# Performance work log

Measured on AMD Instinct MI355X. Metric: run time of the kernel, lower is better.

Reference implementation:

```python
import jax, jax.numpy as jnp
import numpy as np


def setup_inputs() -> dict:
    key = jax.random.key(0)
    k1, k2, k3 = jax.random.split(key, 3)
    B, Cin, Cout, K, H, W = 32, 128, 128, 4, 112, 112
    x = jax.random.normal(k1, (B, Cin, H, W), dtype=jnp.float32)
    # Conv2d 1x1 weights: [K, out_ch, in_ch] (kernel dims of size 1 squeezed)
    expert_w = jax.random.normal(k2, (K, Cout, Cin), dtype=jnp.float32) * (1.0 / np.sqrt(Cin))
    gate_w = jax.random.normal(k3, (K, Cin), dtype=jnp.float32) * (1.0 / np.sqrt(Cin))
    gate_b = jnp.zeros((K,), dtype=jnp.float32)
    return {"x": x, "expert_w": expert_w, "gate_w": gate_w, "gate_b": gate_b}


def reference(x, expert_w, gate_w, gate_b):
    # Gate: global average pool -> 1x1 conv -> softmax over K
    pooled = jnp.mean(x, axis=(2, 3))                      # [B, Cin]
    logits = pooled @ gate_w.T + gate_b                    # [B, K]
    g = jax.nn.softmax(logits, axis=1)                     # [B, K]
    # Combine expert weights per sample (math-equivalent to sum_k g_k * conv_k(x))
    w_b = jnp.einsum('bk,koi->boi', g, expert_w)           # [B, Cout, Cin]
    out = jnp.einsum('boi,bihw->bohw', w_b, x)             # [B, Cout, H, W]
    return out
```

## Files before the change

### kernel.cpp

```cpp
#include <hip/hip_runtime.h>
#include <hip/hip_bf16.h>
#include <stdint.h>

#define B_    32
#define CIN   128
#define COUT  128
#define KEXP  4
#define HW_   12544

typedef __attribute__((ext_vector_type(8))) short bf16x8;
typedef __attribute__((ext_vector_type(4))) float f32x4;

static __device__ __forceinline__ ushort f2bf(float f) {
    uint32_t u = __builtin_bit_cast(uint32_t, f);
    u += 0x7FFFu + ((u >> 16) & 1u);
    return (ushort)(u >> 16);
}

__global__ __launch_bounds__(256) void pool_kernel(const float* __restrict__ x,
                                                   float* __restrict__ pooled) {
    const int row = blockIdx.x;
    const float4* __restrict__ x4 = (const float4*)(x + (size_t)row * HW_);
    const int t = threadIdx.x;
    float s = 0.f;
    for (int idx = t; idx < HW_ / 4; idx += 256) {
        float4 v = x4[idx];
        s += (v.x + v.y) + (v.z + v.w);
    }
    #pragma unroll
    for (int off = 32; off > 0; off >>= 1) s += __shfl_down(s, off, 64);
    __shared__ float wsum[4];
    if ((t & 63) == 0) wsum[t >> 6] = s;
    __syncthreads();
    if (t == 0) pooled[row] = (wsum[0] + wsum[1] + wsum[2] + wsum[3]) * (1.0f / HW_);
}

__global__ __launch_bounds__(256) void gate_kernel(const float* __restrict__ pooled,
                                                   const float* __restrict__ gate_w,
                                                   const float* __restrict__ gate_b,
                                                   const float* __restrict__ expert_w,
                                                   short* __restrict__ wmix) {
    const int b = blockIdx.x;
    const int t = threadIdx.x;
    const int wid = t >> 6, lane = t & 63;
    __shared__ float logits[KEXP];
    __shared__ float gsh[KEXP];
    {
        float p0 = pooled[b * CIN + lane];
        float p1 = pooled[b * CIN + 64 + lane];
        float s = p0 * gate_w[wid * CIN + lane] + p1 * gate_w[wid * CIN + 64 + lane];
        #pragma unroll
        for (int off = 32; off > 0; off >>= 1) s += __shfl_down(s, off, 64);
        if (lane == 0) logits[wid] = s + gate_b[wid];
    }
    __syncthreads();
    if (t == 0) {
        float m = fmaxf(fmaxf(logits[0], logits[1]), fmaxf(logits[2], logits[3]));
        float e0 = expf(logits[0] - m), e1 = expf(logits[1] - m);
        float e2 = expf(logits[2] - m), e3 = expf(logits[3] - m);
        float inv = 1.f / (e0 + e1 + e2 + e3);
        gsh[0] = e0 * inv; gsh[1] = e1 * inv; gsh[2] = e2 * inv; gsh[3] = e3 * inv;
    }
    __syncthreads();
    const float g0 = gsh[0], g1 = gsh[1], g2 = gsh[2], g3 = gsh[3];
    for (int idx = t; idx < COUT * CIN; idx += 256) {
        float w = g0 * expert_w[idx]
                + g1 * expert_w[COUT * CIN + idx]
                + g2 * expert_w[2 * COUT * CIN + idx]
                + g3 * expert_w[3 * COUT * CIN + idx];
        wmix[b * COUT * CIN + idx] = (short)f2bf(w);
    }
}

__global__ __launch_bounds__(256) void conv_kernel(const float* __restrict__ x,
                                                   const short* __restrict__ wmix,
                                                   float* __restrict__ out) {
    __shared__ char wlds[COUT * 256];
    __shared__ char xlds[64 * 256];
    const int b  = blockIdx.y;
    const int p0 = blockIdx.x * 64;
    const int t  = threadIdx.x;

    {
        const uint4* __restrict__ wsrc = (const uint4*)(wmix + (size_t)b * COUT * CIN);
        #pragma unroll
        for (int pass = 0; pass < 8; ++pass) {
            int o  = (t >> 4) + pass * 16;
            int i4 = t & 15;
            uint4 v = wsrc[o * 16 + i4];
            int byte = (o * 256 + i4 * 16) ^ ((o & 7) << 4);
            *(uint4*)(wlds + byte) = v;
        }
    }

    {
        const int pg = t & 15;
        const int cg = t >> 4;
        #pragma unroll
        for (int p = 0; p < 2; ++p) {
            const int cin0 = p * 64 + cg * 4;
            const float* xrow = x + (size_t)b * CIN * HW_ + (size_t)cin0 * HW_ + p0 + pg * 4;
            float va[4][4];
            #pragma unroll
            for (int i = 0; i < 4; ++i) {
                float4 v = *(const float4*)(xrow + (size_t)i * HW_);
                va[i][0] = v.x; va[i][1] = v.y; va[i][2] = v.z; va[i][3] = v.w;
            }
            #pragma unroll
            for (int j = 0; j < 4; ++j) {
                const int pix = pg * 4 + j;
                uint32_t lo = (uint32_t)f2bf(va[0][j]) | ((uint32_t)f2bf(va[1][j]) << 16);
                uint32_t hi = (uint32_t)f2bf(va[2][j]) | ((uint32_t)f2bf(va[3][j]) << 16);
                int byte = (pix * 256 + cin0 * 2) ^ ((pix & 7) << 4);
                uint2 w2; w2.x = lo; w2.y = hi;
                *(uint2*)(xlds + byte) = w2;
            }
        }
    }

    const int wave = t >> 6;
    const int lane = t & 63;
    const int n = lane & 15;
    const int h = lane >> 4;

    __syncthreads();

    bf16x8 xfrag[4];
    {
        const int pixl = wave * 16 + n;
        #pragma unroll
        for (int kk = 0; kk < 4; ++kk) {
            int byte = (pixl * 256 + kk * 64 + h * 16) ^ ((pixl & 7) << 4);
            xfrag[kk] = *(const bf16x8*)(xlds + byte);
        }
    }

    f32x4 acc[8];
    #pragma unroll
    for (int ot = 0; ot < 8; ++ot) acc[ot] = (f32x4){0.f, 0.f, 0.f, 0.f};

    #pragma unroll
    for (int kk = 0; kk < 4; ++kk) {
        #pragma unroll
        for (int ot = 0; ot < 8; ++ot) {
            int o = ot * 16 + n;
            int byte = (o * 256 + kk * 64 + h * 16) ^ ((o & 7) << 4);
            bf16x8 wfrag = *(const bf16x8*)(wlds + byte);
            acc[ot] = __builtin_amdgcn_mfma_f32_16x16x32_bf16(xfrag[kk], wfrag, acc[ot], 0, 0, 0);
        }
    }

    float* __restrict__ ob = out + (size_t)b * COUT * HW_ + p0 + wave * 16 + h * 4;
    #pragma unroll
    for (int ot = 0; ot < 8; ++ot) {
        int cout = ot * 16 + n;
        __builtin_nontemporal_store(acc[ot], (f32x4*)(ob + (size_t)cout * HW_));
    }
}

extern "C" void kernel_launch(void* const* d_in, const int* in_sizes, int n_in,
                              void* d_out, int out_size, void* d_ws, size_t ws_size,
                              hipStream_t stream) {
    const float* x        = (const float*)d_in[0];
    const float* expert_w = (const float*)d_in[1];
    const float* gate_w   = (const float*)d_in[2];
    const float* gate_b   = (const float*)d_in[3];
    float* out = (float*)d_out;

    float* pooled = (float*)d_ws;
    short* wmix   = (short*)((char*)d_ws + 16384);

    pool_kernel<<<dim3(B_ * CIN), 256, 0, stream>>>(x, pooled);
    gate_kernel<<<dim3(B_), 256, 0, stream>>>(pooled, gate_w, gate_b, expert_w, wmix);
    conv_kernel<<<dim3(HW_ / 64, B_), 256, 0, stream>>>(x, wmix, out);
}
```

Before: 131.8 us.

## Fuse pooling with bf16 transposed copy of x and feed conv from it

A new prep kernel reads x once, computes per-chunk channel partial sums for the gate, and writes a pixel-major bf16 copy of x. The gate kernel reduces the partials, and the new conv kernel loads bf16 fragments directly from global memory, two 64-pixel halves per block, with a wider LDS swizzle. This replaces the separate pool pass and the in-conv conversion, but it adds a write and read of an intermediate bf16 tensor. It also needs a large workspace, falling back to the old path otherwise.

```diff
diff --git a/kernel.cpp b/kernel.cpp
--- a/kernel.cpp
+++ b/kernel.cpp
@@ -2,11 +2,12 @@
 #include <hip/hip_bf16.h>
 #include <stdint.h>
 
-#define B_    32
-#define CIN   128
-#define COUT  128
-#define KEXP  4
-#define HW_   12544
+#define B_     32
+#define CIN    128
+#define COUT   128
+#define KEXP   4
+#define HW_    12544
+#define NCHUNK 196
 
 typedef __attribute__((ext_vector_type(8))) short bf16x8;
 typedef __attribute__((ext_vector_type(4))) float f32x4;
@@ -16,6 +17,170 @@
     u += 0x7FFFu + ((u >> 16) & 1u);
     return (ushort)(u >> 16);
 }
+
+
+__global__ __launch_bounds__(256) void prep_kernel(const float* __restrict__ x,
+                                                   short* __restrict__ xbf,
+                                                   float* __restrict__ partial) {
+    const int b  = blockIdx.y;
+    const int cx = blockIdx.x;
+    const int p0 = cx * 64;
+    const int t  = threadIdx.x;
+    const int pg  = t & 15;
+    const int cg8 = t >> 4;
+
+    const float* __restrict__ xr = x + (size_t)b * CIN * HW_
+                                 + (size_t)(cg8 * 8) * HW_ + p0 + pg * 4;
+    f32x4 va[8];
+    #pragma unroll
+    for (int i = 0; i < 8; ++i)
+        va[i] = __builtin_nontemporal_load((const f32x4*)(xr + (size_t)i * HW_));
+
+    float ps[8];
+    #pragma unroll
+    for (int i = 0; i < 8; ++i) ps[i] = (va[i][0] + va[i][1]) + (va[i][2] + va[i][3]);
+    #pragma unroll
+    for (int m = 1; m < 16; m <<= 1) {
+        #pragma unroll
+        for (int i = 0; i < 8; ++i) ps[i] += __shfl_xor(ps[i], m, 64);
+    }
+    if (pg == 0) {
+        float* pdst = partial + ((size_t)b * NCHUNK + cx) * CIN + cg8 * 8;
+        f32x4 v0 = {ps[0], ps[1], ps[2], ps[3]};
+        f32x4 v1 = {ps[4], ps[5], ps[6], ps[7]};
+        *(f32x4*)pdst = v0;
+        *(f32x4*)(pdst + 4) = v1;
+    }
+
+    short* __restrict__ xd = xbf + (size_t)b * HW_ * CIN + (size_t)p0 * CIN + cg8 * 8;
+    #pragma unroll
+    for (int j = 0; j < 4; ++j) {
+        bf16x8 pk;
+        #pragma unroll
+        for (int i = 0; i < 8; ++i) pk[i] = (short)f2bf(va[i][j]);
+        *(bf16x8*)(xd + (size_t)(pg * 4 + j) * CIN) = pk;
+    }
+}
+
+__global__ __launch_bounds__(256) void gate2_kernel(const float* __restrict__ partial,
+                                                    const float* __restrict__ gate_w,
+                                                    const float* __restrict__ gate_b,
+                                                    const float* __restrict__ expert_w,
+                                                    short* __restrict__ wmix) {
+    const int b = blockIdx.x;
+    const int t = threadIdx.x;
+    __shared__ float pl[CIN];
+    if (t < CIN) {
+        float s = 0.f;
+        const float* pp = partial + (size_t)b * NCHUNK * CIN + t;
+        for (int c = 0; c < NCHUNK; ++c) s += pp[(size_t)c * CIN];
+        pl[t] = s * (1.0f / HW_);
+    }
+    __syncthreads();
+
+    const int wid = t >> 6, lane = t & 63;
+    __shared__ float logits[KEXP];
+    __shared__ float gsh[KEXP];
+    {
+        float s = pl[lane] * gate_w[wid * CIN + lane]
+                + pl[64 + lane] * gate_w[wid * CIN + 64 + lane];
+        #pragma unroll
+        for (int off = 32; off > 0; off >>= 1) s += __shfl_down(s, off, 64);
+        if (lane == 0) logits[wid] = s + gate_b[wid];
+    }
+    __syncthreads();
+    if (t == 0) {
+        float m = fmaxf(fmaxf(logits[0], logits[1]), fmaxf(logits[2], logits[3]));
+        float e0 = expf(logits[0] - m), e1 = expf(logits[1] - m);
+        float e2 = expf(logits[2] - m), e3 = expf(logits[3] - m);
+        float inv = 1.f / (e0 + e1 + e2 + e3);
+        gsh[0] = e0 * inv; gsh[1] = e1 * inv; gsh[2] = e2 * inv; gsh[3] = e3 * inv;
+    }
+    __syncthreads();
+    const float g0 = gsh[0], g1 = gsh[1], g2 = gsh[2], g3 = gsh[3];
+    for (int idx = t; idx < COUT * CIN; idx += 256) {
+        float w = g0 * expert_w[idx]
+                + g1 * expert_w[COUT * CIN + idx]
+                + g2 * expert_w[2 * COUT * CIN + idx]
+                + g3 * expert_w[3 * COUT * CIN + idx];
+        wmix[b * COUT * CIN + idx] = (short)f2bf(w);
+    }
+}
+
+__global__ __launch_bounds__(256, 4) void conv2_kernel(const short* __restrict__ xbf,
+                                                       const short* __restrict__ wmix,
+                                                       float* __restrict__ out) {
+    __shared__ char wlds[COUT * 256];
+    const int b   = blockIdx.y;
+    const int t   = threadIdx.x;
+    const int px0 = blockIdx.x * 128;
+
+    {
+        const uint4* __restrict__ wsrc = (const uint4*)(wmix + (size_t)b * COUT * CIN);
+        #pragma unroll
+        for (int pass = 0; pass < 8; ++pass) {
+            int o  = (t >> 4) + pass * 16;
+            int i4 = t & 15;
+            uint4 v = wsrc[o * 16 + i4];
+            *(uint4*)(wlds + o * 256 + ((i4 ^ (o & 15)) << 4)) = v;
+        }
+    }
+
+    const int wave = t >> 6;
+    const int lane = t & 63;
+    const int n = lane & 15;
+    const int h = lane >> 4;
+
+    const short* __restrict__ xb = xbf + (size_t)b * HW_ * CIN
+                                 + (size_t)(px0 + wave * 16 + n) * CIN + h * 8;
+
+    bf16x8 xa[4], xc[4];
+    #pragma unroll
+    for (int kk = 0; kk < 4; ++kk) xa[kk] = *(const bf16x8*)(xb + kk * 32);
+    #pragma unroll
+    for (int kk = 0; kk < 4; ++kk) xc[kk] = *(const bf16x8*)(xb + 64 * CIN + kk * 32);
+
+    __syncthreads();
+
+    f32x4 acc[8];
+
+    #pragma unroll
+    for (int ot = 0; ot < 8; ++ot) acc[ot] = (f32x4){0.f, 0.f, 0.f, 0.f};
+    #pragma unroll
+    for (int ot = 0; ot < 8; ++ot) {
+        const int o = ot * 16 + n;
+        #pragma unroll
+        for (int kk = 0; kk < 4; ++kk) {
+            bf16x8 wfrag = *(const bf16x8*)(wlds + o * 256 + (((kk * 4 + h) ^ n) << 4));
+            acc[ot] = __builtin_amdgcn_mfma_f32_16x16x32_bf16(xa[kk], wfrag, acc[ot], 0, 0, 0);
+        }
+    }
+    {
+        float* __restrict__ ob = out + (size_t)b * COUT * HW_ + px0 + wave * 16 + h * 4;
+        #pragma unroll
+        for (int ot = 0; ot < 8; ++ot)
+            __builtin_nontemporal_store(acc[ot], (f32x4*)(ob + (size_t)(ot * 16 + n) * HW_));
+    }
+
+    #pragma unroll
+    for (int ot = 0; ot < 8; ++ot) acc[ot] = (f32x4){0.f, 0.f, 0.f, 0.f};
+    #pragma unroll
+    for (int ot = 0; ot < 8; ++ot) {
+        const int o = ot * 16 + n;
+        #pragma unroll
+        for (int kk = 0; kk < 4; ++kk) {
+            bf16x8 wfrag = *(const bf16x8*)(wlds + o * 256 + (((kk * 4 + h) ^ n) << 4));
+            acc[ot] = __builtin_amdgcn_mfma_f32_16x16x32_bf16(xc[kk], wfrag, acc[ot], 0, 0, 0);
+        }
+    }
+    {
+        float* __restrict__ ob = out + (size_t)b * COUT * HW_ + px0 + 64 + wave * 16 + h * 4;
+        #pragma unroll
+        for (int ot = 0; ot < 8; ++ot)
+            __builtin_nontemporal_store(acc[ot], (f32x4*)(ob + (size_t)(ot * 16 + n) * HW_));
+    }
+}
+
 
 __global__ __launch_bounds__(256) void pool_kernel(const float* __restrict__ x,
                                                    float* __restrict__ pooled) {
@@ -72,9 +237,9 @@
     }
 }
 
-__global__ __launch_bounds__(256) void conv_kernel(const float* __restrict__ x,
-                                                   const short* __restrict__ wmix,
-                                                   float* __restrict__ out) {
+__global__ __launch_bounds__(256, 4) void conv_fb_kernel(const float* __restrict__ x,
+                                                         const short* __restrict__ wmix,
+                                                         float* __restrict__ out) {
     __shared__ char wlds[COUT * 256];
     __shared__ char xlds[64 * 256];
     const int b  = blockIdx.y;
@@ -88,11 +253,9 @@
             int o  = (t >> 4) + pass * 16;
             int i4 = t & 15;
             uint4 v = wsrc[o * 16 + i4];
-            int byte = (o * 256 + i4 * 16) ^ ((o & 7) << 4);
-            *(uint4*)(wlds + byte) = v;
-        }
-    }
-
+            *(uint4*)(wlds + o * 256 + ((i4 ^ (o & 15)) << 4)) = v;
+        }
+    }
     {
         const int pg = t & 15;
         const int cg = t >> 4;
@@ -140,22 +303,19 @@
     for (int ot = 0; ot < 8; ++ot) acc[ot] = (f32x4){0.f, 0.f, 0.f, 0.f};
 
     #pragma unroll
-    for (int kk = 0; kk < 4; ++kk) {
-        #pragma unroll
-        for (int ot = 0; ot < 8; ++ot) {
-            int o = ot * 16 + n;
-            int byte = (o * 256 + kk * 64 + h * 16) ^ ((o & 7) << 4);
-            bf16x8 wfrag = *(const bf16x8*)(wlds + byte);
+    for (int ot = 0; ot < 8; ++ot) {
+        const int o = ot * 16 + n;
+        #pragma unroll
+        for (int kk = 0; kk < 4; ++kk) {
+            bf16x8 wfrag = *(const bf16x8*)(wlds + o * 256 + (((kk * 4 + h) ^ n) << 4));
             acc[ot] = __builtin_amdgcn_mfma_f32_16x16x32_bf16(xfrag[kk], wfrag, acc[ot], 0, 0, 0);
         }
     }
 
     float* __restrict__ ob = out + (size_t)b * COUT * HW_ + p0 + wave * 16 + h * 4;
     #pragma unroll
-    for (int ot = 0; ot < 8; ++ot) {
-        int cout = ot * 16 + n;
-        __builtin_nontemporal_store(acc[ot], (f32x4*)(ob + (size_t)cout * HW_));
-    }
+    for (int ot = 0; ot < 8; ++ot)
+        __builtin_nontemporal_store(acc[ot], (f32x4*)(ob + (size_t)(ot * 16 + n) * HW_));
 }
 
 extern "C" void kernel_launch(void* const* d_in, const int* in_sizes, int n_in,
@@ -167,10 +327,24 @@
     const float* gate_b   = (const float*)d_in[3];
     float* out = (float*)d_out;
 
-    float* pooled = (float*)d_ws;
-    short* wmix   = (short*)((char*)d_ws + 16384);
-
-    pool_kernel<<<dim3(B_ * CIN), 256, 0, stream>>>(x, pooled);
-    gate_kernel<<<dim3(B_), 256, 0, stream>>>(pooled, gate_w, gate_b, expert_w, wmix);
-    conv_kernel<<<dim3(HW_ / 64, B_), 256, 0, stream>>>(x, wmix, out);
-}
+    const size_t PARTIAL_B = (size_t)B_ * NCHUNK * CIN * 4;
+    const size_t WMIX_B    = (size_t)B_ * COUT * CIN * 2;
+    const size_t XBF_B     = (size_t)B_ * HW_ * CIN * 2;
+    const size_t NEED      = PARTIAL_B + WMIX_B + XBF_B;
+
+    if (ws_size >= NEED) {
+        float* partial = (float*)d_ws;
+        short* wmix    = (short*)((char*)d_ws + PARTIAL_B);
+        short* xbf     = (short*)((char*)d_ws + PARTIAL_B + WMIX_B);
+
+        prep_kernel<<<dim3(NCHUNK, B_), 256, 0, stream>>>(x, xbf, partial);
+        gate2_kernel<<<dim3(B_), 256, 0, stream>>>(partial, gate_w, gate_b, expert_w, wmix);
+        conv2_kernel<<<dim3(HW_ / 128, B_), 256, 0, stream>>>(xbf, wmix, out);
+    } else {
+        float* pooled = (float*)d_ws;
+        short* wmix   = (short*)((char*)d_ws + 16384);
+        pool_kernel<<<dim3(B_ * CIN), 256, 0, stream>>>(x, pooled);
+        gate_kernel<<<dim3(B_), 256, 0, stream>>>(pooled, gate_w, gate_b, expert_w, wmix);
+        conv_fb_kernel<<<dim3(HW_ / 64, B_), 256, 0, stream>>>(x, wmix, out);
+    }
+}
```

New measurement: 142.1 us. 1.08x slower.
